# Kernel optimization log

Hardware: AMD Instinct MI355X
Metric: run time of the kernel (lower is better)

## Reference

```python
import jax, jax.numpy as jnp
import numpy as np

N, E, D, H, L, T = 50000, 200000, 128, 64, 2, 4
SIB_ID = 1
EPS = 1e-6


def _log_map_zero(x, c):
    # x: [N, D+1] on hyperboloid of curvature c; returns [N, D] tangent at origin.
    sqrt_c = jnp.sqrt(c)
    x0 = jnp.clip(sqrt_c * x[..., 0], 1.0 + 1e-7, None)
    dist = jnp.arccosh(x0) / sqrt_c                      # [N]
    sp = x[..., 1:]                                      # [N, D]
    nrm = jnp.maximum(jnp.linalg.norm(sp, axis=-1), EPS)
    return sp * (dist / nrm)[..., None]


def _exp_map_zero(v, c):
    # v: [N, D] tangent at origin; returns [N, D+1] on hyperboloid.
    sqrt_c = jnp.sqrt(c)
    nrm = jnp.maximum(jnp.linalg.norm(v, axis=-1), EPS)  # [N]
    th = sqrt_c * nrm
    x0 = jnp.cosh(th) / sqrt_c
    sp = v * (jnp.sinh(th) / (sqrt_c * nrm))[..., None]
    return jnp.concatenate([x0[..., None], sp], axis=-1)


def setup_inputs() -> dict:
    key = jax.random.key(0)
    ks = jax.random.split(key, 12)
    v0 = 0.1 * jax.random.normal(ks[0], (N, D), dtype=jnp.float32)
    x_hyp = _exp_map_zero(v0, 1.0)
    edge_index = jax.random.randint(ks[1], (2, E), 0, N, dtype=jnp.int32)
    edge_types = jax.random.randint(ks[2], (E,), 0, T, dtype=jnp.int32)
    edge_weights = jax.random.uniform(ks[3], (E,), dtype=jnp.float32) + 0.1
    s_lin = 1.0 / np.sqrt(D)
    s_w1 = 1.0 / np.sqrt(3 * D)
    s_w2 = 1.0 / np.sqrt(H)
    return {
        "x_hyp": x_hyp,
        "edge_index": edge_index,
        "edge_types": edge_types,
        "edge_weights": edge_weights,
        "lin_w": s_lin * jax.random.normal(ks[4], (L, D, D), dtype=jnp.float32),
        "lin_b": jnp.zeros((L, D), dtype=jnp.float32),
        "ln_g": jnp.ones((L, D), dtype=jnp.float32),
        "ln_b": jnp.zeros((L, D), dtype=jnp.float32),
        "edge_emb": 0.02 * jax.random.normal(ks[5], (L, T, D), dtype=jnp.float32),
        "attn_w1": s_w1 * jax.random.normal(ks[6], (L, 3 * D, H), dtype=jnp.float32),
        "attn_b1": jnp.zeros((L, H), dtype=jnp.float32),
        "attn_w2": s_w2 * jax.random.normal(ks[7], (L, H, 1), dtype=jnp.float32),
        "attn_b2": jnp.zeros((L, 1), dtype=jnp.float32),
        "sibling_boost": jnp.full((L,), 0.15, dtype=jnp.float32),
        "curvature": jnp.ones((L,), dtype=jnp.float32),
    }


def _layer(x_hyp, edge_index, edge_types, edge_weights,
           lin_w, lin_b, ln_g, ln_b, emb, w1, b1, w2, b2, sib, curv):
    n = x_hyp.shape[0]
    # curvature is read via .item() in the original -> detached constant
    c = jax.lax.stop_gradient(jnp.clip(curv, 0.1, 10.0))
    x_tan = _log_map_zero(x_hyp, c)                      # [N, D]
    x_lin = x_tan @ lin_w.T + lin_b                      # [N, D]
    src, dst = edge_index[0], edge_index[1]              # PyG: x_j=src, x_i=dst
    x_i = x_lin[dst]                                     # [E, D]
    x_j = x_lin[src]                                     # [E, D]
    e_emb = emb[edge_types]                              # [E, D]
    attn_in = jnp.concatenate([x_i, x_j, e_emb], axis=-1)  # [E, 3D]
    h = jax.nn.silu(attn_in @ w1 + b1)                   # [E, H]
    score = (h @ w2 + b2)[..., 0]                        # [E]
    score = score + jnp.log(jnp.clip(edge_weights, EPS, None))
    score = score + (edge_types == SIB_ID).astype(score.dtype) * sib
    # segment softmax over destination nodes
    seg_max = jax.ops.segment_max(score, dst, num_segments=n)
    ex = jnp.exp(score - seg_max[dst])
    seg_sum = jax.ops.segment_sum(ex, dst, num_segments=n)
    alpha = ex / (seg_sum[dst] + 1e-16)                  # [E]
    msg = (x_j + e_emb) * (alpha * edge_weights)[:, None]  # [E, D]
    x_agg = jax.ops.segment_sum(msg, dst, num_segments=n)  # [N, D]
    x_out = x_tan + x_agg                                # dropout is identity in eval
    mu = jnp.mean(x_out, axis=-1, keepdims=True)
    var = jnp.var(x_out, axis=-1, keepdims=True)
    x_out = (x_out - mu) * jax.lax.rsqrt(var + 1e-5) * ln_g + ln_b
    return _exp_map_zero(x_out, c)


def reference(x_hyp, edge_index, edge_types, edge_weights, lin_w, lin_b,
              ln_g, ln_b, edge_emb, attn_w1, attn_b1, attn_w2, attn_b2,
              sibling_boost, curvature):
    for i in range(lin_w.shape[0]):
        x_hyp = _layer(x_hyp, edge_index, edge_types, edge_weights,
                       lin_w[i], lin_b[i], ln_g[i], ln_b[i], edge_emb[i],
                       attn_w1[i], attn_b1[i], attn_w2[i], attn_b2[i],
                       sibling_boost[i], curvature[i])
    return x_hyp
```

## Files before the change

### kernel.cpp

```cpp
#include <hip/hip_runtime.h>
#include <math.h>

#define WAVE 64
#define KMAX 32

typedef __attribute__((ext_vector_type(8))) short bf16x8;
typedef __attribute__((ext_vector_type(4))) float f32x4;

__device__ __forceinline__ unsigned short f2b(float f) {
    unsigned u = __float_as_uint(f);
    unsigned r = (u + 0x7FFFu + ((u >> 16) & 1u)) >> 16;
    return (unsigned short)r;
}
__device__ __forceinline__ float b2f(unsigned short u) {
    return __uint_as_float(((unsigned)u) << 16);
}
__device__ __forceinline__ float frcp(float x)   { return __builtin_amdgcn_rcpf(x); }
__device__ __forceinline__ float frsq(float x)   { return __builtin_amdgcn_rsqf(x); }
__device__ __forceinline__ float fsqrt2(float x) { return __builtin_amdgcn_sqrtf(x); }
__device__ __forceinline__ float silu(float x)   { return x * frcp(1.f + __expf(-x)); }
__device__ __forceinline__ float facosh(float x) { return __logf(x + fsqrt2(x * x - 1.f)); }

__device__ __forceinline__ void dual_gemm_16(
    unsigned short* sm,
    const unsigned short* __restrict__ LW, const unsigned short* __restrict__ WT,
    const float* __restrict__ bias,
    unsigned short* __restrict__ xlin, unsigned short* __restrict__ acat,
    int base, int N, int tid)
{
    int wave = tid >> 6;
    int lane = tid & 63;
    int quad = lane >> 4;
    int l16  = lane & 15;
    int nloc = tid >> 4;

    __syncthreads();

    bf16x8 a[4];
    #pragma unroll
    for (int kk = 0; kk < 4; ++kk)
        a[kk] = *(const bf16x8*)&sm[l16 * 136 + kk * 32 + quad * 8];

    f32x4 acc[2];
    acc[0] = (f32x4){0.f, 0.f, 0.f, 0.f};
    acc[1] = (f32x4){0.f, 0.f, 0.f, 0.f};
    #pragma unroll
    for (int kk = 0; kk < 4; ++kk) {
        #pragma unroll
        for (int t = 0; t < 2; ++t) {
            int nt = wave * 2 + t;
            bf16x8 b = *(const bf16x8*)&LW[(size_t)(nt * 16 + l16) * 128 + kk * 32 + quad * 8];
            acc[t] = __builtin_amdgcn_mfma_f32_16x16x32_bf16(a[kk], b, acc[t], 0, 0, 0);
        }
    }
    __syncthreads();
    #pragma unroll
    for (int t = 0; t < 2; ++t) {
        int nt = wave * 2 + t;
        float bv = bias[nt * 16 + l16];
        #pragma unroll
        for (int r = 0; r < 4; ++r)
            sm[(quad * 4 + r) * 136 + nt * 16 + l16] = f2b(acc[t][r] + bv);
    }
    __syncthreads();

    bf16x8 a2[4];
    #pragma unroll
    for (int kk = 0; kk < 4; ++kk)
        a2[kk] = *(const bf16x8*)&sm[l16 * 136 + kk * 32 + quad * 8];
    int node = base + nloc;
    if (node < N)
        *(bf16x8*)&xlin[(size_t)node * 128 + 8 * l16] =
            *(const bf16x8*)&sm[nloc * 136 + 8 * l16];

    f32x4 acc2[2];
    acc2[0] = (f32x4){0.f, 0.f, 0.f, 0.f};
    acc2[1] = (f32x4){0.f, 0.f, 0.f, 0.f};
    #pragma unroll
    for (int kk = 0; kk < 4; ++kk) {
        #pragma unroll
        for (int t = 0; t < 2; ++t) {
            int nt = wave * 2 + t;
            bf16x8 b = *(const bf16x8*)&WT[(size_t)(nt * 16 + l16) * 128 + kk * 32 + quad * 8];
            acc2[t] = __builtin_amdgcn_mfma_f32_16x16x32_bf16(a2[kk], b, acc2[t], 0, 0, 0);
        }
    }
    #pragma unroll
    for (int t = 0; t < 2; ++t) {
        int nt = wave * 2 + t;
        #pragma unroll
        for (int r = 0; r < 4; ++r) {
            int rr = base + quad * 4 + r;
            if (rr < N) acat[(size_t)rr * 128 + nt * 16 + l16] = f2b(acc2[t][r]);
        }
    }
}

__global__ __launch_bounds__(256) void k_pre(
    const float* __restrict__ lin_w, const float* __restrict__ w1,
    const float* __restrict__ b1, const float* __restrict__ emb,
    unsigned short* __restrict__ lw_bf, unsigned short* __restrict__ Wt_bf,
    float* __restrict__ ae, int* __restrict__ deg, int N, int PB)
{
    int bid = blockIdx.x, tid = threadIdx.x;
    if (bid < PB) {
        int l = bid / 129, bx = bid % 129;
        const float* lwl = lin_w + (size_t)l * 16384;
        const float* w1l = w1 + (size_t)l * 384 * 64;
        if (bx < 64) {
            int idx = bx * 256 + tid;
            lw_bf[l * 16384 + idx] = f2b(lwl[idx]);
        } else if (bx < 128) {
            int idx = (bx - 64) * 256 + tid;
            int o = idx >> 7, i = idx & 127;
            float v = (o < 64) ? w1l[i * 64 + o] : w1l[(128 + i) * 64 + (o - 64)];
            Wt_bf[l * 16384 + idx] = f2b(v);
        } else {
            int t = tid >> 6, h = tid & 63;
            float s = b1[l * 64 + h];
            #pragma unroll 8
            for (int i = 0; i < 128; ++i)
                s += emb[l * 512 + t * 128 + i] * w1l[(256 + i) * 64 + h];
            ae[l * 256 + tid] = s;
        }
    } else {
        int i0 = ((bid - PB) * 256 + tid) * 4;
        if (i0 + 3 < N) {
            *(int4*)&deg[i0] = make_int4(0, 0, 0, 0);
        } else {
            #pragma unroll
            for (int k2 = 0; k2 < 4; ++k2)
                if (i0 + k2 < N) deg[i0 + k2] = 0;
        }
    }
}

__global__ __launch_bounds__(256) void k_main(
    const int* __restrict__ ei, const int* __restrict__ et,
    const float* __restrict__ ew, const float* __restrict__ xh,
    const float* __restrict__ curv,
    const unsigned short* __restrict__ LW, const unsigned short* __restrict__ WT,
    const float* __restrict__ lb,
    int* __restrict__ deg, int2* __restrict__ epack,
    float* __restrict__ xtf,
    unsigned short* __restrict__ xlin, unsigned short* __restrict__ acat,
    int E, int N, int ECH)
{
    __shared__ __align__(16) unsigned short sm[16 * 136];
    int bid = blockIdx.x, tid = threadIdx.x;
    if (bid < ECH) {
        int e = bid * 256 + tid;
        if (e < E) {
            int dst = ei[E + e];
            int rank = atomicAdd(&deg[dst], 1);
            if (rank < KMAX) {
                int2 r;
                r.x = ei[e] | (et[e] << 24);
                r.y = __float_as_int(ew[e]);
                epack[(size_t)dst * KMAX + rank] = r;
            }
        }
        return;
    }
    int base = (bid - ECH) * 16;
    int l16  = tid & 15;
    int nloc = tid >> 4;
    int node = base + nloc;
    int nodec = node < N ? node : N - 1;

    float c = fminf(fmaxf(curv[0], 0.1f), 10.f);
    float sqc = fsqrt2(c);
    const float* row = xh + (size_t)nodec * 129;
    float x0 = row[0];
    float v[8];
    #pragma unroll
    for (int j = 0; j < 8; ++j) v[j] = row[1 + 8 * l16 + j];
    float n2 = 0.f;
    #pragma unroll
    for (int j = 0; j < 8; ++j) n2 += v[j] * v[j];
    #pragma unroll
    for (int m = 1; m < 16; m <<= 1) n2 += __shfl_xor(n2, m, WAVE);
    float nrm = fmaxf(fsqrt2(n2), 1e-6f);
    float x0c = fmaxf(sqc * x0, 1.f + 1e-7f);
    float f = facosh(x0c) * frcp(sqc) * frcp(nrm);

    float vf[8];
    bf16x8 o8;
    #pragma unroll
    for (int j = 0; j < 8; ++j) {
        vf[j] = v[j] * f;
        o8[j] = (short)f2b(vf[j]);
    }
    if (node < N) {
        *(float4*)&xtf[(size_t)node * 128 + 8 * l16]     = make_float4(vf[0], vf[1], vf[2], vf[3]);
        *(float4*)&xtf[(size_t)node * 128 + 8 * l16 + 4] = make_float4(vf[4], vf[5], vf[6], vf[7]);
    }
    *(bf16x8*)&sm[nloc * 136 + 8 * l16] = o8;

    dual_gemm_16(sm, LW, WT, lb, xlin, acat, base, N, tid);
}

__global__ __launch_bounds__(256) void k_B(
    const int* __restrict__ deg, const int2* __restrict__ epack,
    const unsigned short* __restrict__ acat, const unsigned short* __restrict__ xlin,
    float* __restrict__ xtf, const float* __restrict__ ae,
    const float* __restrict__ emb, const float* __restrict__ w2,
    const float* __restrict__ b2, const float* __restrict__ sib,
    const float* __restrict__ g, const float* __restrict__ b,
    const float* __restrict__ curv, const float* __restrict__ curv_n,
    int last, float* __restrict__ out, int N,
    const unsigned short* __restrict__ LWn, const unsigned short* __restrict__ WTn,
    const float* __restrict__ lbn,
    unsigned short* __restrict__ xlin_o, unsigned short* __restrict__ acat_o)
{
    __shared__ __align__(16) unsigned short sm[16 * 136];
    int tid = threadIdx.x;
    int lane = tid & 63;
    int quad = lane >> 4;
    int l16  = lane & 15;
    int gw = (blockIdx.x * 256 + tid) >> 6;
    int wid = gw * 4 + quad;
    bool nv = wid < N;
    int widc = nv ? wid : N - 1;

    int dg = deg[widc];
    const int4* bp = (const int4*)(epack + (size_t)widc * KMAX);
    int4 myent = bp[l16];
    float4 xt0 = *(const float4*)&xtf[(size_t)widc * 128 + 8 * l16];
    float4 xt1 = *(const float4*)&xtf[(size_t)widc * 128 + 8 * l16 + 4];
    ushort4 adu = *(const ushort4*)&acat[(size_t)widc * 128 + 4 * l16];
    float4 w2v = *(const float4*)&w2[4 * l16];

    float c = fminf(fmaxf(curv[0], 0.1f), 10.f);
    float sqc = fsqrt2(c);
    float rsqc = frcp(sqc);
    dg = dg < KMAX ? dg : KMAX;
    dg = nv ? dg : 0;

    float ad0 = b2f(adu.x), ad1 = b2f(adu.y), ad2 = b2f(adu.z), ad3 = b2f(adu.w);
    float b2v = b2[0], sibv = sib[0];

    float acc[8];
    #pragma unroll
    for (int j = 0; j < 8; ++j) acc[j] = 0.f;
    float S = 0.f;
    float4 St = make_float4(0.f, 0.f, 0.f, 0.f);

    int jm = dg;
    jm = max(jm, __shfl_xor(jm, 16, WAVE));
    jm = max(jm, __shfl_xor(jm, 32, WAVE));
    int jmax = (jm + 1) >> 1;

    ushort4 asuA_n, asuB_n; bf16x8 xuA_n, xuB_n; float4 avA_n, avB_n;
    float wA_n = 1.f, wB_n = 1.f; int tA_n = 0, tB_n = 0;
    bool eA_n = false, eB_n = false;

#define FETCHP(J) {                                                           \
        int lsrc = (quad << 4) + (J);                                         \
        int r0x = __shfl(myent.x, lsrc, WAVE);                                \
        int r0y = __shfl(myent.y, lsrc, WAVE);                                \
        int r1x = __shfl(myent.z, lsrc, WAVE);                                \
        int r1y = __shfl(myent.w, lsrc, WAVE);                                \
        eA_n = (2 * (J)) < dg;                                                \
        eB_n = (2 * (J) + 1) < dg;                                            \
        int sA = eA_n ? (r0x & 0xFFFFFF) : 0;                                 \
        int sB = eB_n ? (r1x & 0xFFFFFF) : 0;                                 \
        tA_n = eA_n ? (int)(((unsigned)r0x) >> 24) : 0;                       \
        tB_n = eB_n ? (int)(((unsigned)r1x) >> 24) : 0;                       \
        wA_n = eA_n ? __int_as_float(r0y) : 1.f;                              \
        wB_n = eB_n ? __int_as_float(r1y) : 1.f;                              \
        asuA_n = *(const ushort4*)&acat[(size_t)sA * 128 + 64 + 4 * l16];     \
        asuB_n = *(const ushort4*)&acat[(size_t)sB * 128 + 64 + 4 * l16];     \
        avA_n  = *(const float4*)&ae[tA_n * 64 + 4 * l16];                    \
        avB_n  = *(const float4*)&ae[tB_n * 64 + 4 * l16];                    \
        xuA_n  = *(const bf16x8*)&xlin[(size_t)sA * 128 + 8 * l16];           \
        xuB_n  = *(const bf16x8*)&xlin[(size_t)sB * 128 + 8 * l16];           \
    }

    if (jmax > 0) FETCHP(0);
    for (int j = 0; j < jmax; ++j) {
        ushort4 asuA = asuA_n, asuB = asuB_n;
        bf16x8 xuA = xuA_n, xuB = xuB_n;
        float4 avA = avA_n, avB = avB_n;
        float wA = wA_n, wB = wB_n;
        int tA = tA_n, tB = tB_n;
        bool eA = eA_n, eB = eB_n;
        if (j + 1 < jmax) FETCHP(j + 1);

        float dA = silu(ad0 + b2f(asuA.x) + avA.x) * w2v.x
                 + silu(ad1 + b2f(asuA.y) + avA.y) * w2v.y
                 + silu(ad2 + b2f(asuA.z) + avA.z) * w2v.z
                 + silu(ad3 + b2f(asuA.w) + avA.w) * w2v.w;
        float dB = silu(ad0 + b2f(asuB.x) + avB.x) * w2v.x
                 + silu(ad1 + b2f(asuB.y) + avB.y) * w2v.y
                 + silu(ad2 + b2f(asuB.z) + avB.z) * w2v.z
                 + silu(ad3 + b2f(asuB.w) + avB.w) * w2v.w;
        #pragma unroll
        for (int m = 1; m < 16; m <<= 1) {
            dA += __shfl_xor(dA, m, WAVE);
            dB += __shfl_xor(dB, m, WAVE);
        }
        float sA = dA + b2v + __logf(fmaxf(wA, 1e-6f));
        if (tA == 1) sA += sibv;
        float exA = eA ? __expf(sA) : 0.f;
        S += exA;
        float cfA = exA * wA;

        float sB2 = dB + b2v + __logf(fmaxf(wB, 1e-6f));
        if (tB == 1) sB2 += sibv;
        float exB = eB ? __expf(sB2) : 0.f;
        S += exB;
        float cfB = exB * wB;

        #pragma unroll
        for (int k = 0; k < 8; ++k)
            acc[k] += b2f((unsigned short)xuA[k]) * cfA;
        #pragma unroll
        for (int k = 0; k < 8; ++k)
            acc[k] += b2f((unsigned short)xuB[k]) * cfB;
        St.x += (tA == 0) ? cfA : 0.f;
        St.y += (tA == 1) ? cfA : 0.f;
        St.z += (tA == 2) ? cfA : 0.f;
        St.w += (tA == 3) ? cfA : 0.f;
        St.x += (tB == 0) ? cfB : 0.f;
        St.y += (tB == 1) ? cfB : 0.f;
        St.z += (tB == 2) ? cfB : 0.f;
        St.w += (tB == 3) ? cfB : 0.f;
    }
#undef FETCHP

    #pragma unroll
    for (int tt = 0; tt < 4; ++tt) {
        float stv = (tt == 0) ? St.x : (tt == 1) ? St.y : (tt == 2) ? St.z : St.w;
        float4 em0 = *(const float4*)&emb[tt * 128 + 8 * l16];
        float4 em1 = *(const float4*)&emb[tt * 128 + 8 * l16 + 4];
        acc[0] += em0.x * stv; acc[1] += em0.y * stv;
        acc[2] += em0.z * stv; acc[3] += em0.w * stv;
        acc[4] += em1.x * stv; acc[5] += em1.y * stv;
        acc[6] += em1.z * stv; acc[7] += em1.w * stv;
    }

    float inv = frcp(S + 1e-16f);
    float y[8];
    y[0] = xt0.x + acc[0] * inv;
    y[1] = xt0.y + acc[1] * inv;
    y[2] = xt0.z + acc[2] * inv;
    y[3] = xt0.w + acc[3] * inv;
    y[4] = xt1.x + acc[4] * inv;
    y[5] = xt1.y + acc[5] * inv;
    y[6] = xt1.z + acc[6] * inv;
    y[7] = xt1.w + acc[7] * inv;

    float sum = 0.f, sq = 0.f;
    #pragma unroll
    for (int j = 0; j < 8; ++j) { sum += y[j]; sq += y[j] * y[j]; }
    #pragma unroll
    for (int m = 1; m < 16; m <<= 1) {
        sum += __shfl_xor(sum, m, WAVE);
        sq  += __shfl_xor(sq, m, WAVE);
    }
    float mu = sum * (1.f / 128.f);
    float var = sq * (1.f / 128.f) - mu * mu;
    float invs = frsq(var + 1e-5f);
    float4 g0 = *(const float4*)&g[8 * l16];
    float4 g1 = *(const float4*)&g[8 * l16 + 4];
    float4 bb0 = *(const float4*)&b[8 * l16];
    float4 bb1 = *(const float4*)&b[8 * l16 + 4];
    y[0] = (y[0] - mu) * invs * g0.x + bb0.x;
    y[1] = (y[1] - mu) * invs * g0.y + bb0.y;
    y[2] = (y[2] - mu) * invs * g0.z + bb0.z;
    y[3] = (y[3] - mu) * invs * g0.w + bb0.w;
    y[4] = (y[4] - mu) * invs * g1.x + bb1.x;
    y[5] = (y[5] - mu) * invs * g1.y + bb1.y;
    y[6] = (y[6] - mu) * invs * g1.z + bb1.z;
    y[7] = (y[7] - mu) * invs * g1.w + bb1.w;

    float nrm2 = 0.f;
    #pragma unroll
    for (int j = 0; j < 8; ++j) nrm2 += y[j] * y[j];
    #pragma unroll
    for (int m = 1; m < 16; m <<= 1) nrm2 += __shfl_xor(nrm2, m, WAVE);
    float nrm = fmaxf(fsqrt2(nrm2), 1e-6f);
    float th = sqc * nrm;
    float e = __expf(th);
    float einv = frcp(e);
    float ch = 0.5f * (e + einv);
    float sh = 0.5f * (e - einv);
    float sc = sh * frcp(sqc * nrm);

    if (last) {
        if (nv) {
            float* o = out + (size_t)wid * 129;
            if (l16 == 0) o[0] = ch * rsqc;
            #pragma unroll
            for (int j = 0; j < 8; ++j) o[1 + 8 * l16 + j] = y[j] * sc;
        }
    } else {
        float x0 = ch * rsqc;
        float c2 = fminf(fmaxf(curv_n[0], 0.1f), 10.f);
        float sqc2 = fsqrt2(c2);
        float x0c = fmaxf(sqc2 * x0, 1.f + 1e-7f);
        float dist = facosh(x0c) * frcp(sqc2);
        float nsp = fmaxf(sh * rsqc, 1e-6f);
        float sf = sc * dist * frcp(nsp);
        float tf[8];
        bf16x8 o8;
        #pragma unroll
        for (int j = 0; j < 8; ++j) {
            tf[j] = y[j] * sf;
            o8[j] = (short)f2b(tf[j]);
        }
        if (nv) {
            *(float4*)&xtf[(size_t)wid * 128 + 8 * l16]     = make_float4(tf[0], tf[1], tf[2], tf[3]);
            *(float4*)&xtf[(size_t)wid * 128 + 8 * l16 + 4] = make_float4(tf[4], tf[5], tf[6], tf[7]);
        }
        *(bf16x8*)&sm[(tid >> 4) * 136 + 8 * l16] = o8;
        dual_gemm_16(sm, LWn, WTn, lbn, xlin_o, acat_o, blockIdx.x * 16, N, tid);
    }
}

extern "C" void kernel_launch(void* const* d_in, const int* in_sizes, int n_in,
                              void* d_out, int out_size, void* d_ws, size_t ws_size,
                              hipStream_t stream) {
    const float* x_hyp = (const float*)d_in[0];
    const int*   ei    = (const int*)d_in[1];
    const int*   et    = (const int*)d_in[2];
    const float* ew    = (const float*)d_in[3];
    const float* lin_w = (const float*)d_in[4];
    const float* lin_b = (const float*)d_in[5];
    const float* ln_g  = (const float*)d_in[6];
    const float* ln_b  = (const float*)d_in[7];
    const float* emb   = (const float*)d_in[8];
    const float* w1    = (const float*)d_in[9];
    const float* b1    = (const float*)d_in[10];
    const float* w2    = (const float*)d_in[11];
    const float* b2    = (const float*)d_in[12];
    const float* sib   = (const float*)d_in[13];
    const float* curv  = (const float*)d_in[14];
    float* out = (float*)d_out;

    const int N = in_sizes[0] / 129;
    const int E = in_sizes[2];
    const int L = in_sizes[4] / (128 * 128);
    const int ECH = (E + 255) / 256;
    const int NB16 = (N + 15) / 16;
    const int PB = L * 129;
    const int ZB = (N + 1023) / 1024;

    float* xtf = (float*)d_ws;
    unsigned short* xlin0 = (unsigned short*)(xtf + (size_t)N * 128);
    unsigned short* acat0 = xlin0 + (size_t)N * 128;
    unsigned short* xlin1 = acat0 + (size_t)N * 128;
    unsigned short* acat1 = xlin1 + (size_t)N * 128;
    int2* epack = (int2*)(acat1 + (size_t)N * 128);
    unsigned short* lw_bf = (unsigned short*)(epack + (size_t)N * KMAX);
    unsigned short* Wt_bf = lw_bf + (size_t)L * 16384;
    float* ae   = (float*)(Wt_bf + (size_t)L * 16384);
    int* deg    = (int*)(ae + (size_t)L * 256);

    k_pre<<<PB + ZB, 256, 0, stream>>>(lin_w, w1, b1, emb,
                                       lw_bf, Wt_bf, ae, deg, N, PB);

    k_main<<<ECH + NB16, 256, 0, stream>>>(
        ei, et, ew, x_hyp, curv, lw_bf, Wt_bf, lin_b,
        deg, epack, xtf, xlin0, acat0, E, N, ECH);

    for (int l = 0; l < L; ++l) {
        int ln = (l + 1 < L) ? l + 1 : l;
        unsigned short* xin = (l & 1) ? xlin1 : xlin0;
        unsigned short* ain = (l & 1) ? acat1 : acat0;
        unsigned short* xot = (l & 1) ? xlin0 : xlin1;
        unsigned short* aot = (l & 1) ? acat0 : acat1;
        k_B<<<NB16, 256, 0, stream>>>(
            deg, epack, ain, xin, xtf,
            ae + (size_t)l * 256, emb + (size_t)l * 512,
            w2 + (size_t)l * 64, b2 + l, sib + l,
            ln_g + (size_t)l * 128, ln_b + (size_t)l * 128,
            curv + l, curv + ln,
            l == L - 1 ? 1 : 0, out, N,
            lw_bf + (size_t)ln * 16384, Wt_bf + (size_t)ln * 16384,
            lin_b + (size_t)ln * 128, xot, aot);
    }
}
```

Before: 222.5 us.

## Fuse all stages into one persistent cooperative kernel with grid syncs

Replaces the separate preprocessing, main and per-layer launches with a single cooperative persistent kernel. Blocks loop over work items and use grid-wide syncs between phases. The first-layer tangent map is now staged through a new bf16 buffer so the GEMM can run after the weight conversion in the same launch. This removes per-launch overhead and inter-kernel gaps, but adds grid-sync cost, limits parallelism to the resident block count, and makes the work loop serialise per block.

```diff
diff --git a/kernel.cpp b/kernel.cpp
--- a/kernel.cpp
+++ b/kernel.cpp
@@ -1,5 +1,8 @@
 #include <hip/hip_runtime.h>
+#include <hip/hip_cooperative_groups.h>
 #include <math.h>
+
+namespace cg = cooperative_groups;
 
 #define WAVE 64
 #define KMAX 32
@@ -21,6 +24,18 @@
 __device__ __forceinline__ float silu(float x)   { return x * frcp(1.f + __expf(-x)); }
 __device__ __forceinline__ float facosh(float x) { return __logf(x + fsqrt2(x * x - 1.f)); }
 
+struct KP {
+    const float* x_hyp; const int* ei; const int* et; const float* ew;
+    const float* lin_w; const float* lin_b; const float* ln_g; const float* ln_b;
+    const float* emb; const float* w1; const float* b1; const float* w2; const float* b2;
+    const float* sib; const float* curv;
+    float* out;
+    float* xtf; unsigned short* xtan_bf;
+    unsigned short* xlin0; unsigned short* acat0; unsigned short* xlin1; unsigned short* acat1;
+    int2* epack; unsigned short* lw_bf; unsigned short* Wt_bf; float* ae; int* deg;
+    int E, N, L, ECH, NT, PB, ZB;
+};
+
 __device__ __forceinline__ void dual_gemm_16(
     unsigned short* sm,
     const unsigned short* __restrict__ LW, const unsigned short* __restrict__ WT,
@@ -96,138 +111,35 @@
     }
 }
 
-__global__ __launch_bounds__(256) void k_pre(
-    const float* __restrict__ lin_w, const float* __restrict__ w1,
-    const float* __restrict__ b1, const float* __restrict__ emb,
-    unsigned short* __restrict__ lw_bf, unsigned short* __restrict__ Wt_bf,
-    float* __restrict__ ae, int* __restrict__ deg, int N, int PB)
-{
-    int bid = blockIdx.x, tid = threadIdx.x;
-    if (bid < PB) {
-        int l = bid / 129, bx = bid % 129;
-        const float* lwl = lin_w + (size_t)l * 16384;
-        const float* w1l = w1 + (size_t)l * 384 * 64;
-        if (bx < 64) {
-            int idx = bx * 256 + tid;
-            lw_bf[l * 16384 + idx] = f2b(lwl[idx]);
-        } else if (bx < 128) {
-            int idx = (bx - 64) * 256 + tid;
-            int o = idx >> 7, i = idx & 127;
-            float v = (o < 64) ? w1l[i * 64 + o] : w1l[(128 + i) * 64 + (o - 64)];
-            Wt_bf[l * 16384 + idx] = f2b(v);
-        } else {
-            int t = tid >> 6, h = tid & 63;
-            float s = b1[l * 64 + h];
-            #pragma unroll 8
-            for (int i = 0; i < 128; ++i)
-                s += emb[l * 512 + t * 128 + i] * w1l[(256 + i) * 64 + h];
-            ae[l * 256 + tid] = s;
-        }
-    } else {
-        int i0 = ((bid - PB) * 256 + tid) * 4;
-        if (i0 + 3 < N) {
-            *(int4*)&deg[i0] = make_int4(0, 0, 0, 0);
-        } else {
-            #pragma unroll
-            for (int k2 = 0; k2 < 4; ++k2)
-                if (i0 + k2 < N) deg[i0 + k2] = 0;
-        }
-    }
-}
-
-__global__ __launch_bounds__(256) void k_main(
-    const int* __restrict__ ei, const int* __restrict__ et,
-    const float* __restrict__ ew, const float* __restrict__ xh,
-    const float* __restrict__ curv,
-    const unsigned short* __restrict__ LW, const unsigned short* __restrict__ WT,
-    const float* __restrict__ lb,
-    int* __restrict__ deg, int2* __restrict__ epack,
-    float* __restrict__ xtf,
-    unsigned short* __restrict__ xlin, unsigned short* __restrict__ acat,
-    int E, int N, int ECH)
-{
-    __shared__ __align__(16) unsigned short sm[16 * 136];
-    int bid = blockIdx.x, tid = threadIdx.x;
-    if (bid < ECH) {
-        int e = bid * 256 + tid;
-        if (e < E) {
-            int dst = ei[E + e];
-            int rank = atomicAdd(&deg[dst], 1);
-            if (rank < KMAX) {
-                int2 r;
-                r.x = ei[e] | (et[e] << 24);
-                r.y = __float_as_int(ew[e]);
-                epack[(size_t)dst * KMAX + rank] = r;
-            }
-        }
-        return;
-    }
-    int base = (bid - ECH) * 16;
-    int l16  = tid & 15;
-    int nloc = tid >> 4;
-    int node = base + nloc;
-    int nodec = node < N ? node : N - 1;
-
-    float c = fminf(fmaxf(curv[0], 0.1f), 10.f);
-    float sqc = fsqrt2(c);
-    const float* row = xh + (size_t)nodec * 129;
-    float x0 = row[0];
-    float v[8];
-    #pragma unroll
-    for (int j = 0; j < 8; ++j) v[j] = row[1 + 8 * l16 + j];
-    float n2 = 0.f;
-    #pragma unroll
-    for (int j = 0; j < 8; ++j) n2 += v[j] * v[j];
-    #pragma unroll
-    for (int m = 1; m < 16; m <<= 1) n2 += __shfl_xor(n2, m, WAVE);
-    float nrm = fmaxf(fsqrt2(n2), 1e-6f);
-    float x0c = fmaxf(sqc * x0, 1.f + 1e-7f);
-    float f = facosh(x0c) * frcp(sqc) * frcp(nrm);
-
-    float vf[8];
-    bf16x8 o8;
-    #pragma unroll
-    for (int j = 0; j < 8; ++j) {
-        vf[j] = v[j] * f;
-        o8[j] = (short)f2b(vf[j]);
-    }
-    if (node < N) {
-        *(float4*)&xtf[(size_t)node * 128 + 8 * l16]     = make_float4(vf[0], vf[1], vf[2], vf[3]);
-        *(float4*)&xtf[(size_t)node * 128 + 8 * l16 + 4] = make_float4(vf[4], vf[5], vf[6], vf[7]);
-    }
-    *(bf16x8*)&sm[nloc * 136 + 8 * l16] = o8;
-
-    dual_gemm_16(sm, LW, WT, lb, xlin, acat, base, N, tid);
-}
-
-__global__ __launch_bounds__(256) void k_B(
-    const int* __restrict__ deg, const int2* __restrict__ epack,
+__device__ void B_tile(
+    unsigned short* sm, const KP& p, int t, int last,
     const unsigned short* __restrict__ acat, const unsigned short* __restrict__ xlin,
-    float* __restrict__ xtf, const float* __restrict__ ae,
-    const float* __restrict__ emb, const float* __restrict__ w2,
-    const float* __restrict__ b2, const float* __restrict__ sib,
-    const float* __restrict__ g, const float* __restrict__ b,
-    const float* __restrict__ curv, const float* __restrict__ curv_n,
-    int last, float* __restrict__ out, int N,
     const unsigned short* __restrict__ LWn, const unsigned short* __restrict__ WTn,
     const float* __restrict__ lbn,
-    unsigned short* __restrict__ xlin_o, unsigned short* __restrict__ acat_o)
+    unsigned short* __restrict__ xlin_o, unsigned short* __restrict__ acat_o,
+    const float* __restrict__ ae, const float* __restrict__ emb,
+    const float* __restrict__ w2, const float* __restrict__ b2,
+    const float* __restrict__ sib, const float* __restrict__ g,
+    const float* __restrict__ b, const float* __restrict__ curv,
+    const float* __restrict__ curv_n)
 {
-    __shared__ __align__(16) unsigned short sm[16 * 136];
     int tid = threadIdx.x;
     int lane = tid & 63;
     int quad = lane >> 4;
     int l16  = lane & 15;
-    int gw = (blockIdx.x * 256 + tid) >> 6;
-    int wid = gw * 4 + quad;
-    bool nv = wid < N;
+    int wv   = tid >> 6;
+    int wid  = t * 16 + wv * 4 + quad;
+    int N    = p.N;
+    bool nv  = wid < N;
     int widc = nv ? wid : N - 1;
 
-    int dg = deg[widc];
-    const int4* bp = (const int4*)(epack + (size_t)widc * KMAX);
+    __syncthreads();
+
+    int dg = p.deg[widc];
+    const int4* bp = (const int4*)(p.epack + (size_t)widc * KMAX);
     int4 myent = bp[l16];
-    float4 xt0 = *(const float4*)&xtf[(size_t)widc * 128 + 8 * l16];
-    float4 xt1 = *(const float4*)&xtf[(size_t)widc * 128 + 8 * l16 + 4];
+    float4 xt0 = *(const float4*)&p.xtf[(size_t)widc * 128 + 8 * l16];
+    float4 xt1 = *(const float4*)&p.xtf[(size_t)widc * 128 + 8 * l16 + 4];
     ushort4 adu = *(const ushort4*)&acat[(size_t)widc * 128 + 4 * l16];
     float4 w2v = *(const float4*)&w2[4 * l16];
 
@@ -390,7 +302,7 @@
 
     if (last) {
         if (nv) {
-            float* o = out + (size_t)wid * 129;
+            float* o = p.out + (size_t)wid * 129;
             if (l16 == 0) o[0] = ch * rsqc;
             #pragma unroll
             for (int j = 0; j < 8; ++j) o[1 + 8 * l16 + j] = y[j] * sc;
@@ -411,74 +323,198 @@
             o8[j] = (short)f2b(tf[j]);
         }
         if (nv) {
-            *(float4*)&xtf[(size_t)wid * 128 + 8 * l16]     = make_float4(tf[0], tf[1], tf[2], tf[3]);
-            *(float4*)&xtf[(size_t)wid * 128 + 8 * l16 + 4] = make_float4(tf[4], tf[5], tf[6], tf[7]);
+            *(float4*)&p.xtf[(size_t)wid * 128 + 8 * l16]     = make_float4(tf[0], tf[1], tf[2], tf[3]);
+            *(float4*)&p.xtf[(size_t)wid * 128 + 8 * l16 + 4] = make_float4(tf[4], tf[5], tf[6], tf[7]);
         }
         *(bf16x8*)&sm[(tid >> 4) * 136 + 8 * l16] = o8;
-        dual_gemm_16(sm, LWn, WTn, lbn, xlin_o, acat_o, blockIdx.x * 16, N, tid);
+        dual_gemm_16(sm, LWn, WTn, lbn, xlin_o, acat_o, t * 16, N, tid);
+    }
+}
+
+__global__ __launch_bounds__(256, 4) void k_all(KP p)
+{
+    __shared__ __align__(16) unsigned short sm[16 * 136];
+    cg::grid_group grid = cg::this_grid();
+    int nb = gridDim.x;
+    int tid = threadIdx.x;
+
+    int tot0 = p.PB + p.ZB + p.NT;
+    for (int w = blockIdx.x; w < tot0; w += nb) {
+        if (w < p.PB) {
+            int l = w / 129, bx = w % 129;
+            const float* lwl = p.lin_w + (size_t)l * 16384;
+            const float* w1l = p.w1 + (size_t)l * 384 * 64;
+            if (bx < 64) {
+                int idx = bx * 256 + tid;
+                p.lw_bf[l * 16384 + idx] = f2b(lwl[idx]);
+            } else if (bx < 128) {
+                int idx = (bx - 64) * 256 + tid;
+                int o = idx >> 7, i = idx & 127;
+                float v = (o < 64) ? w1l[i * 64 + o] : w1l[(128 + i) * 64 + (o - 64)];
+                p.Wt_bf[l * 16384 + idx] = f2b(v);
+            } else {
+                int t = tid >> 6, h = tid & 63;
+                float s = p.b1[l * 64 + h];
+                #pragma unroll 8
+                for (int i = 0; i < 128; ++i)
+                    s += p.emb[l * 512 + t * 128 + i] * w1l[(256 + i) * 64 + h];
+                p.ae[l * 256 + tid] = s;
+            }
+        } else if (w < p.PB + p.ZB) {
+            int i0 = ((w - p.PB) * 256 + tid) * 4;
+            if (i0 + 3 < p.N) {
+                *(int4*)&p.deg[i0] = make_int4(0, 0, 0, 0);
+            } else {
+                #pragma unroll
+                for (int k2 = 0; k2 < 4; ++k2)
+                    if (i0 + k2 < p.N) p.deg[i0 + k2] = 0;
+            }
+        } else {
+            int base = (w - p.PB - p.ZB) * 16;
+            int l16  = tid & 15;
+            int nloc = tid >> 4;
+            int node = base + nloc;
+            int nodec = node < p.N ? node : p.N - 1;
+
+            float c = fminf(fmaxf(p.curv[0], 0.1f), 10.f);
+            float sqc = fsqrt2(c);
+            const float* row = p.x_hyp + (size_t)nodec * 129;
+            float x0 = row[0];
+            float v[8];
+            #pragma unroll
+            for (int j = 0; j < 8; ++j) v[j] = row[1 + 8 * l16 + j];
+            float n2 = 0.f;
+            #pragma unroll
+            for (int j = 0; j < 8; ++j) n2 += v[j] * v[j];
+            #pragma unroll
+            for (int m = 1; m < 16; m <<= 1) n2 += __shfl_xor(n2, m, WAVE);
+            float nrm = fmaxf(fsqrt2(n2), 1e-6f);
+            float x0c = fmaxf(sqc * x0, 1.f + 1e-7f);
+            float f = facosh(x0c) * frcp(sqc) * frcp(nrm);
+
+            float vf[8];
+            bf16x8 o8;
+            #pragma unroll
+            for (int j = 0; j < 8; ++j) {
+                vf[j] = v[j] * f;
+                o8[j] = (short)f2b(vf[j]);
+            }
+            if (node < p.N) {
+                *(float4*)&p.xtf[(size_t)node * 128 + 8 * l16]     = make_float4(vf[0], vf[1], vf[2], vf[3]);
+                *(float4*)&p.xtf[(size_t)node * 128 + 8 * l16 + 4] = make_float4(vf[4], vf[5], vf[6], vf[7]);
+                *(bf16x8*)&p.xtan_bf[(size_t)node * 128 + 8 * l16] = o8;
+            }
+        }
+    }
+    grid.sync();
+
+    int tot1 = p.ECH + p.NT;
+    for (int w = blockIdx.x; w < tot1; w += nb) {
+        if (w < p.ECH) {
+            int e = w * 256 + tid;
+            if (e < p.E) {
+                int dst = p.ei[p.E + e];
+                int rank = atomicAdd(&p.deg[dst], 1);
+                if (rank < KMAX) {
+                    int2 r;
+                    r.x = p.ei[e] | (p.et[e] << 24);
+                    r.y = __float_as_int(p.ew[e]);
+                    p.epack[(size_t)dst * KMAX + rank] = r;
+                }
+            }
+        } else {
+            int t = w - p.ECH;
+            int base = t * 16;
+            int l16  = tid & 15;
+            int nloc = tid >> 4;
+            int node = base + nloc;
+            int nodec = node < p.N ? node : p.N - 1;
+            __syncthreads();
+            *(bf16x8*)&sm[nloc * 136 + 8 * l16] =
+                *(const bf16x8*)&p.xtan_bf[(size_t)nodec * 128 + 8 * l16];
+            dual_gemm_16(sm, p.lw_bf, p.Wt_bf, p.lin_b, p.xlin0, p.acat0,
+                         base, p.N, tid);
+        }
+    }
+    grid.sync();
+
+    for (int l = 0; l < p.L; ++l) {
+        int ln = (l + 1 < p.L) ? l + 1 : l;
+        int last = (l == p.L - 1) ? 1 : 0;
+        const unsigned short* xin = (l & 1) ? p.xlin1 : p.xlin0;
+        const unsigned short* ain = (l & 1) ? p.acat1 : p.acat0;
+        unsigned short* xot = (l & 1) ? p.xlin0 : p.xlin1;
+        unsigned short* aot = (l & 1) ? p.acat0 : p.acat1;
+        for (int t = blockIdx.x; t < p.NT; t += nb)
+            B_tile(sm, p, t, last, ain, xin,
+                   p.lw_bf + (size_t)ln * 16384, p.Wt_bf + (size_t)ln * 16384,
+                   p.lin_b + (size_t)ln * 128, xot, aot,
+                   p.ae + (size_t)l * 256, p.emb + (size_t)l * 512,
+                   p.w2 + (size_t)l * 64, p.b2 + l, p.sib + l,
+                   p.ln_g + (size_t)l * 128, p.ln_b + (size_t)l * 128,
+                   p.curv + l, p.curv + ln);
+        if (!last) grid.sync();
     }
 }
 
 extern "C" void kernel_launch(void* const* d_in, const int* in_sizes, int n_in,
                               void* d_out, int out_size, void* d_ws, size_t ws_size,
                               hipStream_t stream) {
-    const float* x_hyp = (const float*)d_in[0];
-    const int*   ei    = (const int*)d_in[1];
-    const int*   et    = (const int*)d_in[2];
-    const float* ew    = (const float*)d_in[3];
-    const float* lin_w = (const float*)d_in[4];
-    const float* lin_b = (const float*)d_in[5];
-    const float* ln_g  = (const float*)d_in[6];
-    const float* ln_b  = (const float*)d_in[7];
-    const float* emb   = (const float*)d_in[8];
-    const float* w1    = (const float*)d_in[9];
-    const float* b1    = (const float*)d_in[10];
-    const float* w2    = (const float*)d_in[11];
-    const float* b2    = (const float*)d_in[12];
-    const float* sib   = (const float*)d_in[13];
-    const float* curv  = (const float*)d_in[14];
-    float* out = (float*)d_out;
-
-    const int N = in_sizes[0] / 129;
-    const int E = in_sizes[2];
-    const int L = in_sizes[4] / (128 * 128);
-    const int ECH = (E + 255) / 256;
-    const int NB16 = (N + 15) / 16;
-    const int PB = L * 129;
-    const int ZB = (N + 1023) / 1024;
-
-    float* xtf = (float*)d_ws;
-    unsigned short* xlin0 = (unsigned short*)(xtf + (size_t)N * 128);
-    unsigned short* acat0 = xlin0 + (size_t)N * 128;
-    unsigned short* xlin1 = acat0 + (size_t)N * 128;
-    unsigned short* acat1 = xlin1 + (size_t)N * 128;
-    int2* epack = (int2*)(acat1 + (size_t)N * 128);
-    unsigned short* lw_bf = (unsigned short*)(epack + (size_t)N * KMAX);
-    unsigned short* Wt_bf = lw_bf + (size_t)L * 16384;
-    float* ae   = (float*)(Wt_bf + (size_t)L * 16384);
-    int* deg    = (int*)(ae + (size_t)L * 256);
-
-    k_pre<<<PB + ZB, 256, 0, stream>>>(lin_w, w1, b1, emb,
-                                       lw_bf, Wt_bf, ae, deg, N, PB);
-
-    k_main<<<ECH + NB16, 256, 0, stream>>>(
-        ei, et, ew, x_hyp, curv, lw_bf, Wt_bf, lin_b,
-        deg, epack, xtf, xlin0, acat0, E, N, ECH);
-
-    for (int l = 0; l < L; ++l) {
-        int ln = (l + 1 < L) ? l + 1 : l;
-        unsigned short* xin = (l & 1) ? xlin1 : xlin0;
-        unsigned short* ain = (l & 1) ? acat1 : acat0;
-        unsigned short* xot = (l & 1) ? xlin0 : xlin1;
-        unsigned short* aot = (l & 1) ? acat0 : acat1;
-        k_B<<<NB16, 256, 0, stream>>>(
-            deg, epack, ain, xin, xtf,
-            ae + (size_t)l * 256, emb + (size_t)l * 512,
-            w2 + (size_t)l * 64, b2 + l, sib + l,
-            ln_g + (size_t)l * 128, ln_b + (size_t)l * 128,
-            curv + l, curv + ln,
-            l == L - 1 ? 1 : 0, out, N,
-            lw_bf + (size_t)ln * 16384, Wt_bf + (size_t)ln * 16384,
-            lin_b + (size_t)ln * 128, xot, aot);
-    }
+    KP p;
+    p.x_hyp = (const float*)d_in[0];
+    p.ei    = (const int*)d_in[1];
+    p.et    = (const int*)d_in[2];
+    p.ew    = (const float*)d_in[3];
+    p.lin_w = (const float*)d_in[4];
+    p.lin_b = (const float*)d_in[5];
+    p.ln_g  = (const float*)d_in[6];
+    p.ln_b  = (const float*)d_in[7];
+    p.emb   = (const float*)d_in[8];
+    p.w1    = (const float*)d_in[9];
+    p.b1    = (const float*)d_in[10];
+    p.w2    = (const float*)d_in[11];
+    p.b2    = (const float*)d_in[12];
+    p.sib   = (const float*)d_in[13];
+    p.curv  = (const float*)d_in[14];
+    p.out   = (float*)d_out;
+
+    p.N   = in_sizes[0] / 129;
+    p.E   = in_sizes[2];
+    p.L   = in_sizes[4] / (128 * 128);
+    p.ECH = (p.E + 255) / 256;
+    p.NT  = (p.N + 15) / 16;
+    p.PB  = p.L * 129;
+    p.ZB  = (p.N + 1023) / 1024;
+
+    p.xtf = (float*)d_ws;
+    p.xtan_bf = (unsigned short*)(p.xtf + (size_t)p.N * 128);
+    p.xlin0 = p.xtan_bf + (size_t)p.N * 128;
+    p.acat0 = p.xlin0 + (size_t)p.N * 128;
+    p.xlin1 = p.acat0 + (size_t)p.N * 128;
+    p.acat1 = p.xlin1 + (size_t)p.N * 128;
+    p.epack = (int2*)(p.acat1 + (size_t)p.N * 128);
+    p.lw_bf = (unsigned short*)(p.epack + (size_t)p.N * KMAX);
+    p.Wt_bf = p.lw_bf + (size_t)p.L * 16384;
+    p.ae    = (float*)(p.Wt_bf + (size_t)p.L * 16384);
+    p.deg   = (int*)(p.ae + (size_t)p.L * 256);
+
+    static int gridBlocks = 0;
+    if (gridBlocks == 0) {
+        int perCU = 0;
+        hipError_t err = hipOccupancyMaxActiveBlocksPerMultiprocessor(
+            &perCU, k_all, 256, 0);
+        int numCU = 256;
+        hipDeviceProp_t prop;
+        int dev = 0;
+        if (hipGetDevice(&dev) == hipSuccess &&
+            hipGetDeviceProperties(&prop, dev) == hipSuccess)
+            numCU = prop.multiProcessorCount;
+        if (err != hipSuccess || perCU < 1) perCU = 2;
+        gridBlocks = perCU * numCU;
+        if (gridBlocks < 256) gridBlocks = 256;
+    }
+
+    void* args[] = { (void*)&p };
+    hipLaunchCooperativeKernel((void*)k_all, dim3(gridBlocks), dim3(256),
+                               args, 0, stream);
 }
```

After: 522.0 us. 135% more time.
